# Performance work log

Hardware: AMD Instinct MI355X
Metric: run time of the kernel (lower is better)

## Reference

```python
import jax, jax.numpy as jnp
import numpy as np

HEADS = 4
HEAD_DIM = 32
EPS = 1e-12  # torch F.normalize eps


def conv1x1(x, w, b):
    # x: [B, Cin, H, W, D], w: [Cout, Cin], b: [Cout]
    return jnp.einsum('oi,bixyz->boxyz', w, x) + b[None, :, None, None, None]


def split_heads(f):
    # 'b (e c) h w d -> (b e) c w h d'  (note the h<->w swap from the source)
    B, EC, H, W, D = f.shape
    C = EC // HEADS
    f = f.reshape(B, HEADS, C, H, W, D)
    f = f.transpose(0, 1, 2, 4, 3, 5)  # -> [B, E, C, W, H, D]
    return f.reshape(B * HEADS, C, W, H, D)


def adaptive_avg_pool_222(f):
    # AdaptiveAvgPool3d((2,2,2)) with evenly divisible dims == block mean
    B, C, W, H, D = f.shape
    f = f.reshape(B, C, 2, W // 2, 2, H // 2, 2, D // 2)
    return f.mean(axis=(3, 5, 7))  # [B, C, 2, 2, 2]


def l2norm(v):
    n = jnp.linalg.norm(v, axis=-1, keepdims=True)
    return v / jnp.maximum(n, EPS)


def setup_inputs() -> dict:
    key = jax.random.key(0)
    ks = jax.random.split(key, 8)
    B, Cx, S = 2, 64, 40
    EC = HEADS * HEAD_DIM  # 128
    OUT = 256
    def xavier(k, shape, fan_in, fan_out):
        lim = np.sqrt(6.0 / (fan_in + fan_out))
        return jax.random.uniform(k, shape, jnp.float32, -lim, lim)
    return {
        'x': jax.random.normal(ks[0], (B, Cx, S, S, S), jnp.float32),
        'condition': jax.random.normal(ks[1], (B, Cx, S, S, S), jnp.float32),
        'x_enc_w': xavier(ks[2], (EC, Cx), Cx, EC),
        'x_enc_b': jnp.zeros((EC,), jnp.float32),
        'cond_enc_w': xavier(ks[3], (EC, Cx), Cx, EC),
        'cond_enc_b': jnp.zeros((EC,), jnp.float32),
        'sim_alpha': jnp.ones((1,), jnp.float32),
        'sim_beta': jnp.zeros((1,), jnp.float32),
        'proj_w': xavier(ks[4], (OUT, EC), EC, OUT),
        'proj_b': jnp.zeros((OUT,), jnp.float32),
    }


def reference(x, condition, x_enc_w, x_enc_b, cond_enc_w, cond_enc_b,
              sim_alpha, sim_beta, proj_w, proj_b):
    B0 = x.shape[0]
    x_feat = split_heads(conv1x1(x, x_enc_w, x_enc_b))              # [B*E, C, W, H, D]
    cond_feat = split_heads(conv1x1(condition, cond_enc_w, cond_enc_b))
    B, C, W, H, D = x_feat.shape
    N = W * H * D
    M = 8  # 2*2*2 center proposals

    centers = adaptive_avg_pool_222(x_feat).reshape(B, C, M).transpose(0, 2, 1)        # [B, M, C]
    cond_centers = adaptive_avg_pool_222(cond_feat).reshape(B, C, M).transpose(0, 2, 1)  # [B, M, C]
    cond_flat = cond_feat.reshape(B, C, N).transpose(0, 2, 1)        # [B, N, C]

    # cosine sim + affine + sigmoid
    sim = jax.nn.sigmoid(sim_beta + sim_alpha *
                         jnp.einsum('bmc,bnc->bmn', l2norm(centers), l2norm(cond_flat)))  # [B, M, N]

    # hard argmax assignment mask over centers (dim=1), ties -> first idx like torch
    idx = jnp.argmax(sim, axis=1)                                    # [B, N]
    mask = jax.nn.one_hot(idx, M, axis=1, dtype=sim.dtype)           # [B, M, N]
    sim = sim * mask

    # weighted aggregation (einsum == the torch [B,M,N,C] outer-product sum)
    num = jnp.einsum('bmn,bnc->bmc', sim, cond_flat) + cond_centers  # [B, M, C]
    den = sim.sum(axis=-1, keepdims=True) + 1.0                      # [B, M, 1]
    w = num / den                                                    # [B, M, C]
    out = jnp.einsum('bmn,bmc->bnc', sim, w)                         # [B, N, C]

    out = out.transpose(0, 2, 1).reshape(B, C, W, H, D)              # 'b (w h d) c -> b c w h d'
    out = out.reshape(B0, HEADS * C, W, H, D)                        # '(b e) c ... -> b (e c) ...'
    return conv1x1(out, proj_w, proj_b)
```

## Files before the change

kernel.cpp:

```cpp
#include <hip/hip_runtime.h>
#include <math.h>

#define NB0   2
#define CX    64
#define NSP   64000
#define NH    4
#define HD    32
#define NM    8
#define OUTC  256

#define OFF_DMC    0
#define OFF_CC     2048
#define OFF_NUM    4096
#define OFF_DEN    6144
#define OFF_WCT    6208
#define OFF_WXT    14400
#define OFF_CNF    22592
#define OFF_PART   24640
#define OFF_SVAL   843840
#define OFF_SIDX   1355840
#define OFF_PW     1867840

__device__ __forceinline__ float pairwise20(const float* v) {
    float r[8];
    #pragma unroll
    for (int j = 0; j < 8; ++j) r[j] = __fadd_rn(v[j], v[8 + j]);
    float res = __fadd_rn(__fadd_rn(__fadd_rn(r[0], r[1]), __fadd_rn(r[2], r[3])),
                          __fadd_rn(__fadd_rn(r[4], r[5]), __fadd_rn(r[6], r[7])));
    res = __fadd_rn(res, v[16]);
    res = __fadd_rn(res, v[17]);
    res = __fadd_rn(res, v[18]);
    res = __fadd_rn(res, v[19]);
    return res;
}

__device__ __forceinline__ float pairwise32(const float* v) {
    float r[8];
    #pragma unroll
    for (int j = 0; j < 8; ++j)
        r[j] = __fadd_rn(__fadd_rn(__fadd_rn(v[j], v[8 + j]), v[16 + j]), v[24 + j]);
    return __fadd_rn(__fadd_rn(__fadd_rn(r[0], r[1]), __fadd_rn(r[2], r[3])),
                     __fadd_rn(__fadd_rn(r[4], r[5]), __fadd_rn(r[6], r[7])));
}

__device__ __forceinline__ float einsum_dot32(const float* p) {
    float q[16];
    #pragma unroll
    for (int k = 0; k < 4; ++k) {
        #pragma unroll
        for (int l = 0; l < 4; ++l)
            q[k * 4 + l] = __fadd_rn(p[4 * k + l], p[16 + 4 * k + l]);
    }
    float rv[4];
    #pragma unroll
    for (int l = 0; l < 4; ++l)
        rv[l] = __fadd_rn(__fadd_rn(q[l], q[4 + l]), __fadd_rn(q[8 + l], q[12 + l]));
    return __fadd_rn(__fadd_rn(rv[0], rv[2]), __fadd_rn(rv[1], rv[3]));
}

__global__ void transpose_k(const float* __restrict__ cw, const float* __restrict__ xw,
                            float* __restrict__ wct, float* __restrict__ wp4) {
    int idx = blockIdx.x * 256 + threadIdx.x;
    int sel = idx >> 13;
    int j = idx & 8191;
    if (sel == 0) {
        int i = j >> 7, o = j & 127;
        wct[j] = cw[o * 64 + i];
    } else {
        int e = j & 3; int t = j >> 2; int c = t & 31; int i = t >> 5;
        wp4[j] = xw[(e * 32 + c) * 64 + i];
    }
}

__global__ __launch_bounds__(256) void pool_cond_k(const float* __restrict__ cond,
                                                   double* __restrict__ cmean) {
    int bx = blockIdx.x;
    int wh = bx & 3; int hb = wh >> 1; int wb = wh & 1;
    int i   = (bx >> 2) & 63;
    int b0  = bx >> 8;
    const float* src = cond + (size_t)(b0 * CX + i) * NSP + hb * 20 * 1600 + wb * 20 * 40;
    double s0 = 0.0, s1 = 0.0;
    for (int cell = threadIdx.x; cell < 400; cell += 256) {
        int hl = cell / 20, wl = cell - hl * 20;
        const float4* rp = (const float4*)(src + hl * 1600 + wl * 40);
        #pragma unroll
        for (int q = 0; q < 5; ++q) {
            float4 v = rp[q];
            s0 += (double)v.x; s0 += (double)v.y; s0 += (double)v.z; s0 += (double)v.w;
        }
        #pragma unroll
        for (int q = 5; q < 10; ++q) {
            float4 v = rp[q];
            s1 += (double)v.x; s1 += (double)v.y; s1 += (double)v.z; s1 += (double)v.w;
        }
    }
    #pragma unroll
    for (int k = 32; k > 0; k >>= 1) { s0 += __shfl_down(s0, k); s1 += __shfl_down(s1, k); }
    __shared__ double r0[4], r1[4];
    int wid = threadIdx.x >> 6, lane = threadIdx.x & 63;
    if (lane == 0) { r0[wid] = s0; r1[wid] = s1; }
    __syncthreads();
    if (threadIdx.x == 0) {
        double t0 = r0[0] + r0[1] + r0[2] + r0[3];
        double t1 = r1[0] + r1[1] + r1[2] + r1[3];
        double* dst = cmean + b0 * 512 + i * 8 + wb * 4 + hb * 2;
        dst[0] = t0 * (1.0 / 8000.0);
        dst[1] = t1 * (1.0 / 8000.0);
    }
}

__global__ void cc_centers_k(const double* __restrict__ cmean,
                             const float* __restrict__ cw, const float* __restrict__ cb,
                             float* __restrict__ cc) {
    int bx = blockIdx.x;
    int m = bx & 7; int b = bx >> 3; int b0 = b >> 2; int e = b & 3;
    int c = threadIdx.x;
    int o = e * 32 + c;
    double sc = (double)cb[o];
    for (int i = 0; i < 64; ++i)
        sc = fma((double)cw[o * 64 + i], cmean[b0 * 512 + i * 8 + m], sc);
    cc[(b * 8 + m) * 32 + c] = (float)sc;
}

__global__ __launch_bounds__(256, 3) void xfeat_partial_k(
        const float* __restrict__ x, const float* __restrict__ wp4,
        const float* __restrict__ xb, float* __restrict__ partial) {
    __shared__ float xs[512 * 20];
    int bx = blockIdx.x;
    int chunk = bx % 50; int t2 = bx / 50;
    int m  = t2 & 7;
    int b0 = t2 >> 3;
    int qw = m >> 2, qh = (m >> 1) & 1, qd = m & 1;
    int tid = threadIdx.x;
    int lane = tid & 63, wid = tid >> 6;

    const float* xbase = x + (size_t)(b0 * CX) * NSP;
    for (int j = wid; j < 40; j += 4) {
        int slot = j * 64 + lane;
        int row = slot / 5;
        int p   = slot - row * 5;
        int i   = row >> 3;
        int rg  = row & 7;
        int rglob = chunk * 8 + rg;
        int wl = rglob / 20, hl = rglob - wl * 20;
        const float* gp = xbase + (size_t)i * NSP
                        + (qh * 20 + hl) * 1600 + (qw * 20 + wl) * 40 + qd * 20 + p * 4;
        __builtin_amdgcn_global_load_lds(
            (const __attribute__((address_space(1))) void*)gp,
            (__attribute__((address_space(3))) void*)(xs + slot * 4),
            16, 0, 0);
    }
    __syncthreads();

    int c  = tid & 31;
    int rg = tid >> 5;

    float acc[4][20];
    #pragma unroll
    for (int e = 0; e < 4; ++e)
        #pragma unroll
        for (int d = 0; d < 20; ++d) acc[e][d] = 0.f;

    const float* xrow0 = xs + rg * 20;
    for (int i = 0; i < 64; ++i) {
        float4 wv = *(const float4*)(wp4 + ((i * 32 + c) << 2));
        float xv[20];
        #pragma unroll
        for (int dd = 0; dd < 5; ++dd)
            *(float4*)(xv + dd * 4) = *(const float4*)(xrow0 + i * 160 + dd * 4);
        #pragma unroll
        for (int d = 0; d < 20; ++d) {
            acc[0][d] = __fadd_rn(acc[0][d], __fmul_rn(wv.x, xv[d]));
            acc[1][d] = __fadd_rn(acc[1][d], __fmul_rn(wv.y, xv[d]));
            acc[2][d] = __fadd_rn(acc[2][d], __fmul_rn(wv.z, xv[d]));
            acc[3][d] = __fadd_rn(acc[3][d], __fmul_rn(wv.w, xv[d]));
        }
    }

    int rglob = chunk * 8 + rg;
    size_t obase = ((size_t)((b0 * 4) * 8 + m) * 32 + c) * 400 + rglob;
    #pragma unroll
    for (int e = 0; e < 4; ++e) {
        float bias = xb[e * 32 + c];
        float feat[20];
        #pragma unroll
        for (int d = 0; d < 20; ++d) feat[d] = __fadd_rn(acc[e][d], bias);
        partial[obase + (size_t)e * 102400] = pairwise20(feat);
    }
}

__global__ void xcenters_k(const float* __restrict__ partial, float* __restrict__ cnf) {
    int bx = blockIdx.x;
    int c = threadIdx.x;
    const float* pp = partial + ((size_t)(bx * 32 + c)) * 400;
    float acc = 0.f;
    for (int r = 0; r < 400; ++r) acc = __fadd_rn(acc, pp[r]);
    float mean = __fdiv_rn(acc, 8000.0f);
    __shared__ float mm[32];
    mm[c] = mean;
    __syncthreads();
    float sq[32];
    #pragma unroll
    for (int j = 0; j < 32; ++j) sq[j] = __fmul_rn(mm[j], mm[j]);
    float nrm = fmaxf(__fsqrt_rn(pairwise32(sq)), 1e-12f);
    cnf[bx * 32 + c] = __fdiv_rn(mean, nrm);
}

__global__ __launch_bounds__(256) void fused_enc_sim_k(
        const float* __restrict__ cond, const float* __restrict__ wct,
        const float* __restrict__ cnf, const float* __restrict__ cbias,
        const float* __restrict__ alpha_p, const float* __restrict__ beta_p,
        float* __restrict__ sval, int* __restrict__ sidx,
        float* __restrict__ num, float* __restrict__ den) {
    __shared__ float cns[1024];
    __shared__ float agg[1056];
    int tid = threadIdx.x;
    int bx  = blockIdx.x;
    int b0  = bx / 1000;
    int grp = bx - b0 * 1000;
    int sp0 = grp * 64;
    int spL = tid & 63;
    int e = __builtin_amdgcn_readfirstlane(tid >> 6);
    float alpha = alpha_p[0], beta = beta_p[0];
    const float* xcol = cond + (size_t)b0 * CX * NSP + sp0 + spL;
    const float* wt = wct + e * 32;
    const float* bp = cbias + e * 32;
    for (int t = tid; t < 1056; t += 256) agg[t] = 0.f;
    for (int t = tid; t < 1024; t += 256) cns[t] = cnf[b0 * 1024 + t];
    const float* cnp = cns + e * 256;
    __syncthreads();

    float acc[32];
    #pragma unroll
    for (int j = 0; j < 32; ++j) acc[j] = 0.f;
    for (int i = 0; i < 64; ++i) {
        float xv = __ldg(xcol + (size_t)i * NSP);
        const float* wr = wt + i * 128;
        #pragma unroll
        for (int j = 0; j < 32; ++j) acc[j] = __fadd_rn(acc[j], __fmul_rn(wr[j], xv));
    }
    #pragma unroll
    for (int j = 0; j < 32; ++j) acc[j] = __fadd_rn(acc[j], bp[j]);

    float sq[32];
    #pragma unroll
    for (int j = 0; j < 32; ++j) sq[j] = __fmul_rn(acc[j], acc[j]);
    float nrm = fmaxf(__fsqrt_rn(pairwise32(sq)), 1e-12f);
    float u[32];
    #pragma unroll
    for (int j = 0; j < 32; ++j) u[j] = __fdiv_rn(acc[j], nrm);

    float bs = -1.0f; int bi = 0;
    #pragma unroll
    for (int mi = 0; mi < 8; ++mi) {
        float pr[32];
        #pragma unroll
        for (int j = 0; j < 32; ++j) pr[j] = __fmul_rn(cnp[mi * 32 + j], u[j]);
        float dot = einsum_dot32(pr);
        float z = __fadd_rn(beta, __fmul_rn(alpha, dot));
        float sm = (float)(1.0 / (1.0 + exp(-(double)z)));
        if (sm > bs) { bs = sm; bi = mi; }
    }
    float s = bs;

    int sp = sp0 + spL;
    int h = sp / 1600;
    int rem = sp - h * 1600;
    int w = rem / 40;
    int d = rem - w * 40;
    int n = w * 1600 + h * 40 + d;
    int b = b0 * 4 + e;
    sval[b * NSP + n] = s;
    sidx[b * NSP + n] = bi;

    float* al = &agg[(e * 8 + bi) * 32];
    #pragma unroll
    for (int j = 0; j < 32; ++j) atomicAdd(&al[j], s * acc[j]);
    atomicAdd(&agg[1024 + e * 8 + bi], s);

    __syncthreads();
    for (int t = tid; t < 1056; t += 256) {
        float v = agg[t];
        if (t < 1024) atomicAdd(&num[b0 * 1024 + t], v);
        else          atomicAdd(&den[b0 * 32 + (t - 1024)], v);
    }
}

__global__ void wproj_k(const float* __restrict__ num, const float* __restrict__ cc,
                        const float* __restrict__ den, const float* __restrict__ pwm,
                        float* __restrict__ pw_out) {
    int bx = blockIdx.x;
    int b0 = bx >> 8; int o = bx & 255;
    int t = threadIdx.x;
    int e = t >> 3, m = t & 7;
    int b = b0 * 4 + e;
    float dv = den[b * 8 + m] + 1.0f;
    float acc = 0.f;
    for (int c = 0; c < 32; ++c)
        acc = fmaf(pwm[o * 128 + e * 32 + c],
                   num[(b * 8 + m) * 32 + c] + cc[(b * 8 + m) * 32 + c], acc);
    pw_out[(b0 * 256 + o) * 32 + t] = acc / dv;
}

__global__ __launch_bounds__(256) void out_proj_k(
        const float* __restrict__ sval, const int* __restrict__ sidx,
        const float* __restrict__ pw, const float* __restrict__ pb,
        float* __restrict__ out) {
    __shared__ float pwl[4096];
    int tid = threadIdx.x;
    int bx  = blockIdx.x;
    int b0  = bx / 500;
    int r   = bx - b0 * 500;
    int oh  = r / 250;
    int chunk = r - oh * 250;
    int n = chunk * 256 + tid;
    for (int k = 0; k < 16; ++k)
        pwl[k * 256 + tid] = pw[b0 * 8192 + oh * 4096 + k * 256 + tid];
    float s0 = sval[(b0 * 4 + 0) * NSP + n]; int j0 = 0  + sidx[(b0 * 4 + 0) * NSP + n];
    float s1 = sval[(b0 * 4 + 1) * NSP + n]; int j1 = 8  + sidx[(b0 * 4 + 1) * NSP + n];
    float s2 = sval[(b0 * 4 + 2) * NSP + n]; int j2 = 16 + sidx[(b0 * 4 + 2) * NSP + n];
    float s3 = sval[(b0 * 4 + 3) * NSP + n]; int j3 = 24 + sidx[(b0 * 4 + 3) * NSP + n];
    __syncthreads();
    float* ob = out + (size_t)b0 * OUTC * NSP + (size_t)oh * 128 * NSP + n;
    const float* pbh = pb + oh * 128;
    #pragma unroll 4
    for (int o = 0; o < 128; ++o) {
        const float* prw = &pwl[o * 32];
        float v = pbh[o];
        v = fmaf(s0, prw[j0], v);
        v = fmaf(s1, prw[j1], v);
        v = fmaf(s2, prw[j2], v);
        v = fmaf(s3, prw[j3], v);
        ob[(size_t)o * NSP] = v;
    }
}

extern "C" void kernel_launch(void* const* d_in, const int* in_sizes, int n_in,
                              void* d_out, int out_size, void* d_ws, size_t ws_size,
                              hipStream_t stream) {
    const float* x     = (const float*)d_in[0];
    const float* cond  = (const float*)d_in[1];
    const float* xw    = (const float*)d_in[2];
    const float* xb    = (const float*)d_in[3];
    const float* cw    = (const float*)d_in[4];
    const float* cb    = (const float*)d_in[5];
    const float* alpha = (const float*)d_in[6];
    const float* beta  = (const float*)d_in[7];
    const float* pwm   = (const float*)d_in[8];
    const float* pb    = (const float*)d_in[9];
    float* out = (float*)d_out;
    float* wsf = (float*)d_ws;

    double* dmc = (double*)(wsf + OFF_DMC);
    float* cc   = wsf + OFF_CC;
    float* num  = wsf + OFF_NUM;
    float* den  = wsf + OFF_DEN;
    float* wct  = wsf + OFF_WCT;
    float* wp4  = wsf + OFF_WXT;
    float* cnf  = wsf + OFF_CNF;
    float* part = wsf + OFF_PART;
    float* sv   = wsf + OFF_SVAL;
    int*   si   = (int*)(wsf + OFF_SIDX);
    float* pwq  = wsf + OFF_PW;

    hipMemsetAsync(num, 0, (2048 + 64) * sizeof(float), stream);
    transpose_k<<<64, 256, 0, stream>>>(cw, xw, wct, wp4);
    pool_cond_k<<<512, 256, 0, stream>>>(cond, dmc);
    cc_centers_k<<<64, 32, 0, stream>>>(dmc, cw, cb, cc);
    xfeat_partial_k<<<800, 256, 0, stream>>>(x, wp4, xb, part);
    xcenters_k<<<64, 32, 0, stream>>>(part, cnf);
    fused_enc_sim_k<<<2000, 256, 0, stream>>>(cond, wct, cnf, cb, alpha, beta, sv, si, num, den);
    wproj_k<<<512, 32, 0, stream>>>(num, cc, den, pwm, pwq);
    out_proj_k<<<1000, 256, 0, stream>>>(sv, si, pwq, pb, out);
}
```

Baseline: 385.7 us.

## Process two voxels per thread with LDS-staged inputs and packed FP32 math

The fused encoder/similarity kernel now handles 128 spatial positions per block instead of 64, with each thread computing two adjacent voxels. The condition tile is staged into LDS through direct global-to-LDS loads. The 1x1 conv accumulation uses v_pk_mul/v_pk_add on float pairs, which halves weight loads and VALU instruction count per voxel. The LDS buffer is reused for the aggregation scratch, and the block count is halved with a launch-bounds occupancy hint. In exchange, register pressure rises from the doubled accumulators and the per-block LDS footprint grows.

```diff
diff --git a/kernel.cpp b/kernel.cpp
--- a/kernel.cpp
+++ b/kernel.cpp
@@ -8,6 +8,8 @@
 #define HD    32
 #define NM    8
 #define OUTC  256
+
+typedef float f32x2 __attribute__((ext_vector_type(2)));
 
 #define OFF_DMC    0
 #define OFF_CC     2048
@@ -206,77 +208,109 @@
     cnf[bx * 32 + c] = __fdiv_rn(mean, nrm);
 }
 
-__global__ __launch_bounds__(256) void fused_enc_sim_k(
+__global__ __launch_bounds__(256, 3) void fused_enc_sim_k(
         const float* __restrict__ cond, const float* __restrict__ wct,
         const float* __restrict__ cnf, const float* __restrict__ cbias,
         const float* __restrict__ alpha_p, const float* __restrict__ beta_p,
         float* __restrict__ sval, int* __restrict__ sidx,
         float* __restrict__ num, float* __restrict__ den) {
+    __shared__ float xs[8192];
     __shared__ float cns[1024];
-    __shared__ float agg[1056];
     int tid = threadIdx.x;
     int bx  = blockIdx.x;
-    int b0  = bx / 1000;
-    int grp = bx - b0 * 1000;
-    int sp0 = grp * 64;
+    int b0  = bx / 500;
+    int grp = bx - b0 * 500;
+    int sp0 = grp * 128;
     int spL = tid & 63;
+    int lane = tid & 63, wid = tid >> 6;
     int e = __builtin_amdgcn_readfirstlane(tid >> 6);
     float alpha = alpha_p[0], beta = beta_p[0];
-    const float* xcol = cond + (size_t)b0 * CX * NSP + sp0 + spL;
     const float* wt = wct + e * 32;
     const float* bp = cbias + e * 32;
-    for (int t = tid; t < 1056; t += 256) agg[t] = 0.f;
+
+    const float* cbase = cond + (size_t)b0 * CX * NSP + sp0;
+    for (int j = wid; j < 32; j += 4) {
+        int slot = j * 64 + lane;
+        int i  = slot >> 5;
+        int vq = slot & 31;
+        const float* gp = cbase + (size_t)i * NSP + vq * 4;
+        __builtin_amdgcn_global_load_lds(
+            (const __attribute__((address_space(1))) void*)gp,
+            (__attribute__((address_space(3))) void*)(xs + slot * 4),
+            16, 0, 0);
+    }
     for (int t = tid; t < 1024; t += 256) cns[t] = cnf[b0 * 1024 + t];
     const float* cnp = cns + e * 256;
     __syncthreads();
 
-    float acc[32];
-    #pragma unroll
-    for (int j = 0; j < 32; ++j) acc[j] = 0.f;
+    f32x2 acc2[32];
+    #pragma unroll
+    for (int j = 0; j < 32; ++j) { acc2[j].x = 0.f; acc2[j].y = 0.f; }
     for (int i = 0; i < 64; ++i) {
-        float xv = __ldg(xcol + (size_t)i * NSP);
-        const float* wr = wt + i * 128;
-        #pragma unroll
-        for (int j = 0; j < 32; ++j) acc[j] = __fadd_rn(acc[j], __fmul_rn(wr[j], xv));
-    }
-    #pragma unroll
-    for (int j = 0; j < 32; ++j) acc[j] = __fadd_rn(acc[j], bp[j]);
-
-    float sq[32];
-    #pragma unroll
-    for (int j = 0; j < 32; ++j) sq[j] = __fmul_rn(acc[j], acc[j]);
-    float nrm = fmaxf(__fsqrt_rn(pairwise32(sq)), 1e-12f);
-    float u[32];
-    #pragma unroll
-    for (int j = 0; j < 32; ++j) u[j] = __fdiv_rn(acc[j], nrm);
-
-    float bs = -1.0f; int bi = 0;
-    #pragma unroll
-    for (int mi = 0; mi < 8; ++mi) {
-        float pr[32];
-        #pragma unroll
-        for (int j = 0; j < 32; ++j) pr[j] = __fmul_rn(cnp[mi * 32 + j], u[j]);
-        float dot = einsum_dot32(pr);
-        float z = __fadd_rn(beta, __fmul_rn(alpha, dot));
-        float sm = (float)(1.0 / (1.0 + exp(-(double)z)));
-        if (sm > bs) { bs = sm; bi = mi; }
-    }
-    float s = bs;
-
-    int sp = sp0 + spL;
-    int h = sp / 1600;
-    int rem = sp - h * 1600;
-    int w = rem / 40;
-    int d = rem - w * 40;
-    int n = w * 1600 + h * 40 + d;
-    int b = b0 * 4 + e;
-    sval[b * NSP + n] = s;
-    sidx[b * NSP + n] = bi;
-
-    float* al = &agg[(e * 8 + bi) * 32];
-    #pragma unroll
-    for (int j = 0; j < 32; ++j) atomicAdd(&al[j], s * acc[j]);
-    atomicAdd(&agg[1024 + e * 8 + bi], s);
+        f32x2 xv2 = *(const f32x2*)(xs + i * 128 + 2 * spL);
+        const f32x2* wr2 = (const f32x2*)(wt + i * 128);
+        #pragma unroll
+        for (int t = 0; t < 16; ++t) {
+            f32x2 w2 = wr2[t];
+            f32x2 pe, po;
+            asm("v_pk_mul_f32 %0, %1, %2 op_sel:[0,0] op_sel_hi:[0,1]"
+                : "=v"(pe) : "s"(w2), "v"(xv2));
+            asm("v_pk_mul_f32 %0, %1, %2 op_sel:[1,0] op_sel_hi:[1,1]"
+                : "=v"(po) : "s"(w2), "v"(xv2));
+            asm("v_pk_add_f32 %0, %0, %1" : "+v"(acc2[2 * t])     : "v"(pe));
+            asm("v_pk_add_f32 %0, %0, %1" : "+v"(acc2[2 * t + 1]) : "v"(po));
+        }
+    }
+
+    __syncthreads();
+    float* agg = xs;
+    for (int t = tid; t < 1056; t += 256) agg[t] = 0.f;
+    __syncthreads();
+
+    #pragma unroll
+    for (int v = 0; v < 2; ++v) {
+        float a[32];
+        #pragma unroll
+        for (int j = 0; j < 32; ++j) {
+            float h0 = v ? acc2[j].y : acc2[j].x;
+            a[j] = __fadd_rn(h0, bp[j]);
+        }
+        float sq[32];
+        #pragma unroll
+        for (int j = 0; j < 32; ++j) sq[j] = __fmul_rn(a[j], a[j]);
+        float nrm = fmaxf(__fsqrt_rn(pairwise32(sq)), 1e-12f);
+        float u[32];
+        #pragma unroll
+        for (int j = 0; j < 32; ++j) u[j] = __fdiv_rn(a[j], nrm);
+
+        float bs = -1.0f; int bi = 0;
+        #pragma unroll
+        for (int mi = 0; mi < 8; ++mi) {
+            float pr[32];
+            #pragma unroll
+            for (int j = 0; j < 32; ++j) pr[j] = __fmul_rn(cnp[mi * 32 + j], u[j]);
+            float dot = einsum_dot32(pr);
+            float z = __fadd_rn(beta, __fmul_rn(alpha, dot));
+            float sm = (float)(1.0 / (1.0 + exp(-(double)z)));
+            if (sm > bs) { bs = sm; bi = mi; }
+        }
+        float s = bs;
+
+        int sp = sp0 + 2 * spL + v;
+        int h = sp / 1600;
+        int rem = sp - h * 1600;
+        int w = rem / 40;
+        int d = rem - w * 40;
+        int n = w * 1600 + h * 40 + d;
+        int b = b0 * 4 + e;
+        sval[b * NSP + n] = s;
+        sidx[b * NSP + n] = bi;
+
+        float* al = &agg[(e * 8 + bi) * 32];
+        #pragma unroll
+        for (int j = 0; j < 32; ++j) atomicAdd(&al[j], s * a[j]);
+        atomicAdd(&agg[1024 + e * 8 + bi], s);
+    }
 
     __syncthreads();
     for (int t = tid; t < 1056; t += 256) {
@@ -369,7 +403,7 @@
     cc_centers_k<<<64, 32, 0, stream>>>(dmc, cw, cb, cc);
     xfeat_partial_k<<<800, 256, 0, stream>>>(x, wp4, xb, part);
     xcenters_k<<<64, 32, 0, stream>>>(part, cnf);
-    fused_enc_sim_k<<<2000, 256, 0, stream>>>(cond, wct, cnf, cb, alpha, beta, sv, si, num, den);
+    fused_enc_sim_k<<<1000, 256, 0, stream>>>(cond, wct, cnf, cb, alpha, beta, sv, si, num, den);
     wproj_k<<<512, 32, 0, stream>>>(num, cc, den, pwm, pwq);
     out_proj_k<<<1000, 256, 0, stream>>>(sv, si, pwq, pb, out);
 }
```

After: 543.7 us. +40.9%, slower.
